# Kernel optimization log

Measured on AMD Instinct MI355X. Metric: run time of the kernel, lower is better.

Reference implementation:

```python
import jax, jax.numpy as jnp
import numpy as np

B, FIN, H, W = 16, 256, 32, 32
NH, FH = 8, 64
CIN = FIN + 2  # fin + 2 coordinate-grid pos channels
COUT = NH * FH


def setup_inputs() -> dict:
    key = jax.random.key(0)
    ks = jax.random.split(key, 9)
    s = 1.0 / np.sqrt(CIN)
    so = 1.0 / np.sqrt(COUT)
    return {
        "x": jax.random.normal(ks[0], (B, FIN, H, W), dtype=jnp.float32),
        "wq": jax.random.uniform(ks[1], (COUT, CIN), jnp.float32, -s, s),
        "bq": jax.random.uniform(ks[2], (COUT,), jnp.float32, -s, s),
        "wk": jax.random.uniform(ks[3], (COUT, CIN), jnp.float32, -s, s),
        "bk": jax.random.uniform(ks[4], (COUT,), jnp.float32, -s, s),
        "wv": jax.random.uniform(ks[5], (COUT, CIN), jnp.float32, -s, s),
        "bv": jax.random.uniform(ks[6], (COUT,), jnp.float32, -s, s),
        "wo": jax.random.uniform(ks[7], (FIN, COUT), jnp.float32, -so, so),
        "bo": jax.random.uniform(ks[8], (FIN,), jnp.float32, -so, so),
    }


def reference(x, wq, bq, wk, bk, wv, bv, wo, bo):
    b, c, h, w = x.shape
    n = h * w
    # PosEncoding: concat one linspace(-1,1) coordinate channel per spatial dim
    gy, gx = jnp.meshgrid(jnp.linspace(-1.0, 1.0, h), jnp.linspace(-1.0, 1.0, w), indexing="ij")
    pos = jnp.broadcast_to(jnp.stack([gy, gx])[None], (b, 2, h, w)).astype(x.dtype)
    t = jnp.concatenate([x, pos], axis=1).reshape(b, c + 2, n)  # [B, C+2, N]
    # 1x1 convs are per-token GEMMs
    q = (jnp.einsum("oc,bcn->bon", wq, t) + bq[:, None]).reshape(b, NH, FH, n)
    k = (jnp.einsum("oc,bcn->bon", wk, t) + bk[:, None]).reshape(b, NH, FH, n)
    v = (jnp.einsum("oc,bcn->bon", wv, t) + bv[:, None]).reshape(b, NH, FH, n)
    temp = FH ** 0.5
    attn = jax.nn.softmax(jnp.einsum("bhdn,bhdm->bhnm", q, k) / temp, axis=-1)
    o = jnp.einsum("bhnm,bhdm->bhdn", attn, v).reshape(b, NH * FH, n)
    o = jnp.einsum("oc,bcn->bon", wo, o) + bo[:, None]
    return x + o.reshape(b, c, h, w)
```

## Files before the change

kernel.cpp:

```cpp
#include <hip/hip_runtime.h>


typedef unsigned short u16;
typedef unsigned int   u32;
typedef __attribute__((ext_vector_type(8))) short  short8;
typedef __attribute__((ext_vector_type(4))) float  float4_;

#define MFMA16(a, b, c) __builtin_amdgcn_mfma_f32_16x16x32_bf16(a, b, c, 0, 0, 0)

__device__ __forceinline__ float bf2f(u16 u) {
    union { u32 i; float f; } v; v.i = ((u32)u) << 16; return v.f;
}
__device__ __forceinline__ u16 f2bf(float f) {
    union { float f; u32 i; } v; v.f = f;
    u32 r = v.i + 0x7FFFu + ((v.i >> 16) & 1u);
    return (u16)(r >> 16);
}
__device__ __forceinline__ float exp2_fast(float x) {
    float r;
    asm("v_exp_f32 %0, %1" : "=v"(r) : "v"(x));
    return r;
}
__device__ __forceinline__ u32 cvtpk_bf16(float lo, float hi) {
    u32 r;
    asm("v_cvt_pk_bf16_f32 %0, %1, %2" : "=v"(r) : "v"(lo), "v"(hi));
    return r;
}

__global__ __launch_bounds__(256) void prep(
    const float* __restrict__ wq, const float* __restrict__ wk,
    const float* __restrict__ wv, const float* __restrict__ x,
    u16* __restrict__ wb, u16* __restrict__ xT)
{
    __shared__ float Lt[64][65];
    const int bid = blockIdx.x;
    const int tid = threadIdx.x;
    if (bid < 512) {
        int i = bid * 256 + tid;
        int o = i >> 8, c = i & 255;
        size_t si = (size_t)o * 258 + c;
        wb[i]          = f2bf(wq[si]);
        wb[131072 + i] = f2bf(wk[si]);
        wb[262144 + i] = f2bf(wv[si]);
    } else {
        int r = bid - 512;
        int n0 = (r & 15) * 64, c0 = ((r >> 4) & 3) * 64, b = r >> 6;
#pragma unroll
        for (int p = 0; p < 4; ++p) {
            int c = p * 16 + (tid >> 4);
            int nn = (tid & 15) * 4;
            float4 v = *(const float4*)&x[((size_t)(b * 256) + c0 + c) * 1024 + n0 + nn];
            Lt[c][nn + 0] = v.x; Lt[c][nn + 1] = v.y;
            Lt[c][nn + 2] = v.z; Lt[c][nn + 3] = v.w;
        }
        __syncthreads();
#pragma unroll
        for (int p = 0; p < 4; ++p) {
            int n = p * 16 + (tid >> 4);
            int cc = (tid & 15) * 4;
            ushort4 st;
            st.x = f2bf(Lt[cc + 0][n]); st.y = f2bf(Lt[cc + 1][n]);
            st.z = f2bf(Lt[cc + 2][n]); st.w = f2bf(Lt[cc + 3][n]);
            *(ushort4*)&xT[((size_t)(b << 10) + n0 + n) * 256 + c0 + cc] = st;
        }
    }
}

__global__ __launch_bounds__(256) void qkv_mfma(
    const u16* __restrict__ xT, const u16* __restrict__ wb,
    const float* __restrict__ wq, const float* __restrict__ wk,
    const float* __restrict__ wv,
    const float* __restrict__ bq, const float* __restrict__ bk,
    const float* __restrict__ bv,
    u16* __restrict__ qkvbuf)
{
    __shared__ u16 Wl[128 * 64];
    __shared__ u16 Tl[128 * 64];
    const int tid = threadIdx.x;
    const int lane = tid & 63, w = tid >> 6;
    const int quad = lane >> 4, m15 = lane & 15;
    const int n0 = blockIdx.x * 128, mt = blockIdx.y, b = blockIdx.z;
    const int mat = mt >> 2;
    const int m0 = mt * 128;
    const float* worig = (mat == 0) ? wq : ((mat == 1) ? wk : wv);
    const float* bias  = (mat == 0) ? bq : ((mat == 1) ? bk : bv);
    const float oscale = (mat == 1) ? 0.1803368801111204f : 1.0f;
    u16* outbuf = qkvbuf + (size_t)mat * 8388608;

    float4_ acc[2][8];
#pragma unroll
    for (int s = 0; s < 2; ++s)
#pragma unroll
        for (int t = 0; t < 8; ++t) acc[s][t] = (float4_){0, 0, 0, 0};

    const int row = tid >> 3, c8 = (tid & 7) * 8;
    const int stsw = c8 ^ ((row & 7) << 3);
    const int rdsw = (m15 & 7) << 3;

    for (int cc0 = 0; cc0 < 256; cc0 += 64) {
        __syncthreads();
#pragma unroll
        for (int rr = 0; rr < 128; rr += 32) {
            *(short8*)&Wl[(row + rr) * 64 + stsw] =
                *(const short8*)(wb + (size_t)(m0 + row + rr) * 256 + cc0 + c8);
            *(short8*)&Tl[(row + rr) * 64 + stsw] =
                *(const short8*)(xT + ((size_t)(b << 10) + n0 + row + rr) * 256 + cc0 + c8);
        }
        __syncthreads();
#pragma unroll
        for (int c = 0; c < 2; ++c) {
            short8 af[2];
#pragma unroll
            for (int s = 0; s < 2; ++s)
                af[s] = *(const short8*)&Wl[(w * 32 + s * 16 + m15) * 64 +
                                            ((c * 32 + quad * 8) ^ rdsw)];
#pragma unroll
            for (int t = 0; t < 8; ++t) {
                short8 bf = *(const short8*)&Tl[(t * 16 + m15) * 64 +
                                                ((c * 32 + quad * 8) ^ rdsw)];
#pragma unroll
                for (int s = 0; s < 2; ++s)
                    acc[s][t] = MFMA16(af[s], bf, acc[s][t]);
            }
        }
    }

#pragma unroll
    for (int s = 0; s < 2; ++s) {
        float wg[4], wx[4], bi[4];
#pragma unroll
        for (int r = 0; r < 4; ++r) {
            int om = (mt & 3) * 128 + w * 32 + s * 16 + quad * 4 + r;
            wg[r] = worig[(size_t)om * 258 + 256];
            wx[r] = worig[(size_t)om * 258 + 257];
            bi[r] = bias[om];
        }
        const int h = (mt & 3) * 2 + ((w * 32 + s * 16) >> 6);
        const int dbase = ((w * 32 + s * 16) & 63) + quad * 4;
#pragma unroll
        for (int t = 0; t < 8; ++t) {
            int n = n0 + t * 16 + m15;
            float gy = -1.0f + 2.0f * (float)(n >> 5) / 31.0f;
            float gx = -1.0f + 2.0f * (float)(n & 31) / 31.0f;
            float v[4];
#pragma unroll
            for (int r = 0; r < 4; ++r)
                v[r] = (acc[s][t][r] + wg[r] * gy + wx[r] * gx + bi[r]) * oscale;
            if (mat != 2) {
                ushort4 st;
                st.x = f2bf(v[0]); st.y = f2bf(v[1]);
                st.z = f2bf(v[2]); st.w = f2bf(v[3]);
                *(ushort4*)&outbuf[((size_t)(b * 8 + h) * 1024 + n) * 64 + dbase] = st;
            } else {
#pragma unroll
                for (int r = 0; r < 4; ++r)
                    outbuf[((size_t)(b * 8 + h) * 64 + dbase + r) * 1024 + n] = f2bf(v[r]);
            }
        }
    }
}

__global__ __launch_bounds__(512) void attn_mfma(
    u16* __restrict__ qbuf, const u16* __restrict__ kbuf,
    const u16* __restrict__ vbuf)
{
    __shared__ u16 Kl[64 * 64];
    __shared__ u16 Vl[64 * 64];
    __shared__ u16 Pl[8][8][16][8];

    const int tid = threadIdx.x;
    const int lane = tid & 63, w = tid >> 6;
    const int quad = lane >> 4, m15 = lane & 15;
    const int bh = blockIdx.x;
    const int q0 = blockIdx.y * 128;
    u16* qb = qbuf + (size_t)bh * 65536;
    const u16* kb = kbuf + (size_t)bh * 65536;
    const u16* vb = vbuf + (size_t)bh * 65536;

    short8 qf[2];
    {
        const u16* qr = qb + (size_t)(q0 + w * 16 + m15) * 64 + quad * 8;
        qf[0] = *(const short8*)qr;
        qf[1] = *(const short8*)(qr + 32);
    }

    float4_ O[4];
    float lp = 0.0f;
#pragma unroll
    for (int t = 0; t < 4; ++t) O[t] = (float4_){0, 0, 0, 0};

    const int row = tid >> 3, c8 = (tid & 7) * 8;
    const int stsw = c8 ^ ((row & 7) << 3);
    const int rdsw = (m15 & 7) << 3;

    {
        short8 k0 = *(const short8*)(kb + (size_t)row * 64 + c8);
        short8 v0 = *(const short8*)(vb + (size_t)row * 1024 + c8);
        *(short8*)&Kl[row * 64 + stsw] = k0;
        *(short8*)&Vl[row * 64 + stsw] = v0;
    }
    __syncthreads();

    short8 kr, vr;
    for (int kt0 = 0; kt0 < 1024; kt0 += 64) {
        const bool more = (kt0 < 960);
        if (more) {
            kr = *(const short8*)(kb + (size_t)(kt0 + 64 + row) * 64 + c8);
            vr = *(const short8*)(vb + (size_t)row * 1024 + kt0 + 64 + c8);
        }

        float4_ S[4];
#pragma unroll
        for (int t = 0; t < 4; ++t) S[t] = (float4_){0, 0, 0, 0};
#pragma unroll
        for (int c = 0; c < 2; ++c) {
            short8 kf[4];
#pragma unroll
            for (int t = 0; t < 4; ++t)
                kf[t] = *(const short8*)&Kl[(t * 16 + m15) * 64 +
                                            ((c * 32 + quad * 8) ^ rdsw)];
            __builtin_amdgcn_s_setprio(1);
#pragma unroll
            for (int t = 0; t < 4; ++t)
                S[t] = MFMA16(kf[t], qf[c], S[t]);
            __builtin_amdgcn_s_setprio(0);
        }

        {
            float lsum = 0.0f;
#pragma unroll
            for (int t = 0; t < 4; ++t) {
                float p0 = exp2_fast(S[t][0]);
                float p1 = exp2_fast(S[t][1]);
                float p2 = exp2_fast(S[t][2]);
                float p3 = exp2_fast(S[t][3]);
                uint2 st; st.x = cvtpk_bf16(p0, p1); st.y = cvtpk_bf16(p2, p3);
                *(uint2*)&Pl[w][t * 2 + (quad >> 1)][m15][(quad & 1) * 4] = st;
                lsum += (p0 + p1) + (p2 + p3);
            }
            lp += lsum;
        }

#pragma unroll
        for (int c = 0; c < 2; ++c) {
            short8 av[4];
#pragma unroll
            for (int dt = 0; dt < 4; ++dt)
                av[dt] = *(const short8*)&Vl[(dt * 16 + m15) * 64 +
                                             ((c * 32 + quad * 8) ^ rdsw)];
            short8 bp = *(const short8*)&Pl[w][c * 4 + quad][m15][0];
            __builtin_amdgcn_s_setprio(1);
#pragma unroll
            for (int dt = 0; dt < 4; ++dt)
                O[dt] = MFMA16(av[dt], bp, O[dt]);
            __builtin_amdgcn_s_setprio(0);
        }

        __syncthreads();
        if (more) {
            *(short8*)&Kl[row * 64 + stsw] = kr;
            *(short8*)&Vl[row * 64 + stsw] = vr;
            __syncthreads();
        }
    }

    {
        float v = lp;
        v += __shfl_xor(v, 16);
        v += __shfl_xor(v, 32);
        float linv = 1.0f / v;
        int n = q0 + w * 16 + m15;
#pragma unroll
        for (int dt = 0; dt < 4; ++dt) {
            ushort4 st;
            st.x = f2bf(O[dt][0] * linv);
            st.y = f2bf(O[dt][1] * linv);
            st.z = f2bf(O[dt][2] * linv);
            st.w = f2bf(O[dt][3] * linv);
            *(ushort4*)&qb[(size_t)n * 64 + dt * 16 + quad * 4] = st;
        }
    }
}

__global__ __launch_bounds__(256) void proj_mfma(
    const u16* __restrict__ ao, const float* __restrict__ wo,
    const float* __restrict__ bo, const float* __restrict__ x,
    float* __restrict__ out)
{
    __shared__ u16 Wl[64 * 64];
    __shared__ u16 Tl[64 * 64];
    const int tid = threadIdx.x;
    const int lane = tid & 63, w = tid >> 6;
    const int quad = lane >> 4, m15 = lane & 15;
    const int n0 = blockIdx.x * 64, f0 = blockIdx.y * 64, b = blockIdx.z;

    float4_ acc[4] = {{0,0,0,0},{0,0,0,0},{0,0,0,0},{0,0,0,0}};
    const int row = tid >> 3, c8 = (tid & 7) * 8;
    const int stsw = c8 ^ ((row & 7) << 3);
    const int rdsw = (m15 & 7) << 3;

    for (int cc0 = 0; cc0 < 512; cc0 += 64) {
        __syncthreads();
        const int h = cc0 >> 6;
#pragma unroll
        for (int rr = 0; rr < 64; rr += 32) {
            const float* wsrc = wo + (size_t)(f0 + row + rr) * 512 + cc0 + c8;
            float4 v0 = *(const float4*)wsrc;
            float4 v1 = *(const float4*)(wsrc + 4);
            uint4 pk;
            pk.x = cvtpk_bf16(v0.x, v0.y);
            pk.y = cvtpk_bf16(v0.z, v0.w);
            pk.z = cvtpk_bf16(v1.x, v1.y);
            pk.w = cvtpk_bf16(v1.z, v1.w);
            *(uint4*)&Wl[(row + rr) * 64 + stsw] = pk;
            *(short8*)&Tl[(row + rr) * 64 + stsw] =
                *(const short8*)(ao + ((size_t)((b << 3) + h) * 1024 + n0 + row + rr) * 64 + c8);
        }
        __syncthreads();
#pragma unroll
        for (int c = 0; c < 2; ++c) {
            short8 af = *(const short8*)&Wl[(w * 16 + m15) * 64 +
                                            ((c * 32 + quad * 8) ^ rdsw)];
#pragma unroll
            for (int t = 0; t < 4; ++t) {
                short8 bf = *(const short8*)&Tl[(t * 16 + m15) * 64 +
                                                ((c * 32 + quad * 8) ^ rdsw)];
                acc[t] = MFMA16(af, bf, acc[t]);
            }
        }
    }

    float bi[4];
#pragma unroll
    for (int r = 0; r < 4; ++r) bi[r] = bo[f0 + w * 16 + quad * 4 + r];
#pragma unroll
    for (int t = 0; t < 4; ++t) {
        int n = n0 + t * 16 + m15;
#pragma unroll
        for (int r = 0; r < 4; ++r) {
            int f = f0 + w * 16 + quad * 4 + r;
            size_t idx = ((size_t)(b * 256) + f) * 1024 + n;
            out[idx] = acc[t][r] + bi[r] + x[idx];
        }
    }
}

extern "C" void kernel_launch(void* const* d_in, const int* in_sizes, int n_in,
                              void* d_out, int out_size, void* d_ws, size_t ws_size,
                              hipStream_t stream) {
    const float* x  = (const float*)d_in[0];
    const float* wq = (const float*)d_in[1];
    const float* bq = (const float*)d_in[2];
    const float* wk = (const float*)d_in[3];
    const float* bk = (const float*)d_in[4];
    const float* wv = (const float*)d_in[5];
    const float* bv = (const float*)d_in[6];
    const float* wo = (const float*)d_in[7];
    const float* bo = (const float*)d_in[8];

    u16* qkvbuf = (u16*)d_ws;
    u16* region = qkvbuf + 3 * 8388608;
    u16* xT = region;
    u16* wb = region + 4194304;

    prep<<<1536, 256, 0, stream>>>(wq, wk, wv, x, wb, xT);

    qkv_mfma<<<dim3(8, 12, 16), 256, 0, stream>>>(
        xT, wb, wq, wk, wv, bq, bk, bv, qkvbuf);

    attn_mfma<<<dim3(128, 8), 512, 0, stream>>>(
        qkvbuf, qkvbuf + 8388608, qkvbuf + 16777216);

    proj_mfma<<<dim3(16, 4, 16), 256, 0, stream>>>(qkvbuf, wo, bo, x, (float*)d_out);
}
```

Measured before the change: 186.4 us.

## Double-buffer QKV projection K-loop with register prefetch and MFMA priority

Restructures the QKV projection GEMM K-loop into 32-wide chunks and splits the 64-column LDS tiles into two halves used as a double buffer. Global loads for the next chunk go into registers before the MFMAs on the current chunk and are written into the other half afterward, so one barrier per step replaces two. s_setprio raises wave priority around the MFMA block. The goal is to hide global load latency behind compute, at the cost of more barrier steps and extra live registers.

New measurement: 174.3 us. 1.07x faster.

```diff
diff --git a/kernel.cpp b/kernel.cpp
--- a/kernel.cpp
+++ b/kernel.cpp
@@ -93,36 +93,58 @@
 #pragma unroll
         for (int t = 0; t < 8; ++t) acc[s][t] = (float4_){0, 0, 0, 0};
 
-    const int row = tid >> 3, c8 = (tid & 7) * 8;
-    const int stsw = c8 ^ ((row & 7) << 3);
+    const int srow = tid >> 2;
+    const int sc8  = (tid & 3) * 8;
     const int rdsw = (m15 & 7) << 3;
-
-    for (int cc0 = 0; cc0 < 256; cc0 += 64) {
-        __syncthreads();
-#pragma unroll
-        for (int rr = 0; rr < 128; rr += 32) {
-            *(short8*)&Wl[(row + rr) * 64 + stsw] =
-                *(const short8*)(wb + (size_t)(m0 + row + rr) * 256 + cc0 + c8);
-            *(short8*)&Tl[(row + rr) * 64 + stsw] =
-                *(const short8*)(xT + ((size_t)(b << 10) + n0 + row + rr) * 256 + cc0 + c8);
-        }
-        __syncthreads();
-#pragma unroll
-        for (int c = 0; c < 2; ++c) {
-            short8 af[2];
-#pragma unroll
-            for (int s = 0; s < 2; ++s)
-                af[s] = *(const short8*)&Wl[(w * 32 + s * 16 + m15) * 64 +
-                                            ((c * 32 + quad * 8) ^ rdsw)];
-#pragma unroll
-            for (int t = 0; t < 8; ++t) {
-                short8 bf = *(const short8*)&Tl[(t * 16 + m15) * 64 +
-                                                ((c * 32 + quad * 8) ^ rdsw)];
-#pragma unroll
-                for (int s = 0; s < 2; ++s)
-                    acc[s][t] = MFMA16(af[s], bf, acc[s][t]);
-            }
-        }
+    const int sw0  = (srow & 7) << 3;
+
+    const u16* wsrc = wb + (size_t)(m0 + srow) * 256 + sc8;
+    const u16* tsrc = xT + ((size_t)(b << 10) + n0 + srow) * 256 + sc8;
+
+    {
+        short8 w0 = *(const short8*)(wsrc);
+        short8 w1 = *(const short8*)(wsrc + 64 * 256);
+        short8 t0 = *(const short8*)(tsrc);
+        short8 t1 = *(const short8*)(tsrc + 64 * 256);
+        *(short8*)&Wl[srow * 64 + (sc8 ^ sw0)]        = w0;
+        *(short8*)&Wl[(srow + 64) * 64 + (sc8 ^ sw0)] = w1;
+        *(short8*)&Tl[srow * 64 + (sc8 ^ sw0)]        = t0;
+        *(short8*)&Tl[(srow + 64) * 64 + (sc8 ^ sw0)] = t1;
+    }
+    __syncthreads();
+
+#pragma unroll
+    for (int k = 0; k < 8; ++k) {
+        const int p = k & 1;
+        short8 pw0, pw1, pt0, pt1;
+        if (k < 7) {
+            const int kc = (k + 1) * 32;
+            pw0 = *(const short8*)(wsrc + kc);
+            pw1 = *(const short8*)(wsrc + 64 * 256 + kc);
+            pt0 = *(const short8*)(tsrc + kc);
+            pt1 = *(const short8*)(tsrc + 64 * 256 + kc);
+        }
+
+        const int cb = p * 32 + quad * 8;
+        short8 af0 = *(const short8*)&Wl[(w * 32 + m15) * 64 + (cb ^ rdsw)];
+        short8 af1 = *(const short8*)&Wl[(w * 32 + 16 + m15) * 64 + (cb ^ rdsw)];
+        __builtin_amdgcn_s_setprio(1);
+#pragma unroll
+        for (int t = 0; t < 8; ++t) {
+            short8 bf = *(const short8*)&Tl[(t * 16 + m15) * 64 + (cb ^ rdsw)];
+            acc[0][t] = MFMA16(af0, bf, acc[0][t]);
+            acc[1][t] = MFMA16(af1, bf, acc[1][t]);
+        }
+        __builtin_amdgcn_s_setprio(0);
+
+        if (k < 7) {
+            const int pc = (p ^ 1) * 32 + sc8;
+            *(short8*)&Wl[srow * 64 + (pc ^ sw0)]        = pw0;
+            *(short8*)&Wl[(srow + 64) * 64 + (pc ^ sw0)] = pw1;
+            *(short8*)&Tl[srow * 64 + (pc ^ sw0)]        = pt0;
+            *(short8*)&Tl[(srow + 64) * 64 + (pc ^ sw0)] = pt1;
+        }
+        __syncthreads();
     }
 
 #pragma unroll
```
